# Kernel optimization log

Hardware: AMD Instinct MI355X
Metric: run time of the kernel (lower is better)

The kernel has to match this reference:

```python
import jax, jax.numpy as jnp
import numpy as np

B, W, C = 128, 64, 48
NUM_CHARS, E, H, HM, CTX, CTXM, OUT = 256, 64, 128, 128, 128, 128, 8


def _gru(x, lens, Wih, Whh, bih, bhh):
    """Masked unidirectional GRU. x: [N,T,D], lens: [N]. Outputs zero at t>=len
    (matching pad_packed_sequence), state frozen past len."""
    N, T, _ = x.shape
    Hd = Whh.shape[1]
    xg = jnp.einsum('ntd,gd->ntg', x, Wih) + bih  # [N,T,3H] precomputed input gates

    def step(h, inp):
        xg_t, t = inp
        hg = h @ Whh.T + bhh
        xr, xz, xn = jnp.split(xg_t, 3, axis=-1)
        hr, hz, hn = jnp.split(hg, 3, axis=-1)
        r = jax.nn.sigmoid(xr + hr)
        z = jax.nn.sigmoid(xz + hz)
        n = jnp.tanh(xn + r * hn)
        hnew = (1 - z) * n + z * h
        valid = (t < lens)[:, None]
        h2 = jnp.where(valid, hnew, h)
        out = jnp.where(valid, hnew, jnp.zeros_like(hnew))
        return h2, out

    h0 = jnp.zeros((N, Hd), x.dtype)
    _, outs = jax.lax.scan(step, h0, (xg.transpose(1, 0, 2), jnp.arange(T)))
    return outs.transpose(1, 0, 2)  # [N,T,H]


def _rev(x, lens):
    """Reverse each sequence within its valid length; pad positions unchanged."""
    T = x.shape[1]
    t = jnp.arange(T)[None, :]
    idx = jnp.where(t < lens[:, None], lens[:, None] - 1 - t, t)
    return jnp.take_along_axis(x, idx[:, :, None], axis=1)


def _bigru(x, lens, Wf, Uf, bif, bhf, Wb, Ub, bib, bhb):
    of = _gru(x, lens, Wf, Uf, bif, bhf)
    ob = _rev(_gru(_rev(x, lens), lens, Wb, Ub, bib, bhb), lens)
    return jnp.concatenate([of, ob], axis=-1)


def _attn_pool(out, Wp, bp, ctx):
    # out: [N,T,K]; softmax over ALL T positions (pads have out=0, faithful to source)
    proj = jnp.tanh(jnp.einsum('ntk,ck->ntc', out, Wp) + bp)
    att = jax.nn.softmax(proj @ ctx, axis=1)  # [N,T]
    return jnp.einsum('nt,ntk->nk', att, out)


def setup_inputs():
    key = jax.random.key(0)
    ks = iter(jax.random.split(key, 40))
    nrm = lambda shape: jax.random.normal(next(ks), shape, jnp.float32) * 0.1
    chars = jax.random.randint(next(ks), (B, W, C), 0, NUM_CHARS, dtype=jnp.int32)
    lens = jax.random.randint(next(ks), (B, W), 1, C + 1, dtype=jnp.int32)
    inp = dict(chars=chars, lens=lens, emb=nrm((NUM_CHARS, E)))
    for p, din, h in [('c', E, H), ('m', 2 * H, HM)]:
        for d in ('f', 'b'):
            inp[p + 'Wih_' + d] = nrm((3 * h, din))
            inp[p + 'Whh_' + d] = nrm((3 * h, h))
            inp[p + 'bih_' + d] = nrm((3 * h,))
            inp[p + 'bhh_' + d] = nrm((3 * h,))
    inp.update(wWp=nrm((CTX, 2 * H)), wbp=nrm((CTX,)), wctx=nrm((CTX,)),
               pWp=nrm((CTXM, 2 * HM)), pbp=nrm((CTXM,)), pctx=nrm((CTXM,)),
               Wout=nrm((OUT, 2 * HM)), bout=nrm((OUT,)))
    return inp


def reference(chars, lens, emb,
              cWih_f, cWhh_f, cbih_f, cbhh_f, cWih_b, cWhh_b, cbih_b, cbhh_b,
              mWih_f, mWhh_f, mbih_f, mbhh_f, mWih_b, mWhh_b, mbih_b, mbhh_b,
              wWp, wbp, wctx, pWp, pbp, pctx, Wout, bout):
    Bb, Ww, Cc = chars.shape
    x = emb[chars.reshape(Bb * Ww, Cc)]        # [B*W, C, E]
    l = lens.reshape(Bb * Ww)
    char_out = _bigru(x, l, cWih_f, cWhh_f, cbih_f, cbhh_f,
                      cWih_b, cWhh_b, cbih_b, cbhh_b)  # [B*W, C, 2H]
    words = _attn_pool(char_out, wWp, wbp, wctx).reshape(Bb, Ww, -1)  # [B, W, 2H]
    lw = jnp.full((Bb,), Ww, dtype=lens.dtype)
    msg_out = _bigru(words, lw, mWih_f, mWhh_f, mbih_f, mbhh_f,
                     mWih_b, mWhh_b, mbih_b, mbhh_b)  # [B, W, 2HM]
    messages = _attn_pool(msg_out, pWp, pbp, pctx)     # [B, 2HM]
    outputs = messages @ Wout.T + bout                 # [B, OUT]
    return outputs, messages
```

## Files before the change

### kernel.cpp

```cpp
#include <hip/hip_runtime.h>
#include <stdint.h>
#include <stddef.h>

#define NCH   256
#define EDIM  64
#define HDIM  128
#define G3    384
#define BATCH 128
#define WRD   64
#define CLEN  48
#define NW    8192
#define OUTD  8

#define LOG2E 1.44269504088896f

#define C_EMB     0
#define C_CWIH_F  16384
#define C_CWHH_F  40960
#define C_CBIH_F  90112
#define C_CBHH_F  90496
#define C_CWIH_B  90880
#define C_CWHH_B  115456
#define C_CBIH_B  164608
#define C_CBHH_B  164992
#define C_MWIH_F  165376
#define C_MWHH_F  263680
#define C_MBIH_F  312832
#define C_MBHH_F  313600
#define C_MWIH_B  314368
#define C_MWHH_B  412672
#define C_MBIH_B  461824
#define C_MBHH_B  462592
#define C_WWP     463360
#define C_WBP     496128
#define C_WCTX    496256
#define C_PWP     496384
#define C_PBP     529152
#define C_PCTX    529280
#define C_WOUT    529408
#define C_BOUT    531456
#define C_TOTAL   531464

#define OFF_FLAG    0u
#define OFF_CANON   1024u
#define OFF_WPFRAG  (4u*1024u*1024u)
#define OFF_PFRAG   (4u*1024u*1024u + 65536u)
#define OFF_MFRAG   (4u*1024u*1024u + 131072u)
#define OFF_BIASV   (4u*1024u*1024u + 524288u)
#define OFF_XGT4    5111808u
#define OFF_WORDS   35651584u
#define OFF_MSGOUT  47185920u
#define OFF_CHOUT   54525952u

typedef _Float16 h2v __attribute__((ext_vector_type(2)));
typedef _Float16 f16x8 __attribute__((ext_vector_type(8)));
typedef float f32x4 __attribute__((ext_vector_type(4)));

__device__ __forceinline__ float bf16_to_f32(unsigned short u){
  union{unsigned int i;float f;}v; v.i=((unsigned int)u)<<16; return v.f;
}
__device__ __forceinline__ unsigned short f32_to_bf16(float f){
  union{float f;unsigned int i;}v; v.f=f;
  unsigned int u=v.i; unsigned int r=(u + 0x7fffu + ((u>>16)&1u))>>16;
  return (unsigned short)r;
}
__device__ __forceinline__ uint32_t pack_h2(float x,float y){
  h2v h; h[0]=(_Float16)x; h[1]=(_Float16)y; uint32_t u; __builtin_memcpy(&u,&h,4); return u;
}
__device__ __forceinline__ unsigned short f32_to_h16u(float f){
  _Float16 h=(_Float16)f; unsigned short u; __builtin_memcpy(&u,&h,2); return u;
}
__device__ __forceinline__ float dot2(uint32_t a, uint32_t b, float c){
#if __has_builtin(__builtin_amdgcn_fdot2)
  h2v av,bv; __builtin_memcpy(&av,&a,4); __builtin_memcpy(&bv,&b,4);
  return __builtin_amdgcn_fdot2(av,bv,c,false);
#else
  h2v av,bv; __builtin_memcpy(&av,&a,4); __builtin_memcpy(&bv,&b,4);
  return c + (float)av[0]*(float)bv[0] + (float)av[1]*(float)bv[1];
#endif
}
__device__ __forceinline__ float exp2_fast(float x){
#if __has_builtin(__builtin_amdgcn_exp2f)
  return __builtin_amdgcn_exp2f(x);
#else
  return exp2f(x);
#endif
}
__device__ __forceinline__ float rcp_fast(float x){
#if __has_builtin(__builtin_amdgcn_rcpf)
  return __builtin_amdgcn_rcpf(x);
#else
  return 1.f/x;
#endif
}
__device__ __forceinline__ float sig2(float s){ return rcp_fast(1.f+exp2_fast(s)); }
__device__ __forceinline__ float tanh2(float u){ return fmaf(-2.f, rcp_fast(exp2_fast(u)+1.f), 1.f); }
__device__ __forceinline__ float wave_sum(float v){
  #pragma unroll
  for(int m=32;m>=1;m>>=1) v += __shfl_xor(v,m,64);
  return v;
}
__device__ __forceinline__ float wave_max(float v){
  #pragma unroll
  for(int m=32;m>=1;m>>=1) v = fmaxf(v,__shfl_xor(v,m,64));
  return v;
}
__device__ __forceinline__ f32x4 mfma16(f16x8 a, f16x8 b, f32x4 c){
  return __builtin_amdgcn_mfma_f32_16x16x32_f16(a, b, c, 0, 0, 0);
}

struct ConvArgs { const void* src[25]; int len[25]; int off[25]; };

__global__ void k_convert(ConvArgs a, int* __restrict__ flag, float* __restrict__ dst){
  const unsigned short* u=(const unsigned short*)a.src[0];
  int found=0;
  for(int i=threadIdx.x;i<2048;i+=256){ float v=bf16_to_f32(u[i]); if(fabsf(v)>8.f) found=1; }
  __shared__ int s;
  if(threadIdx.x==0) s=0;
  __syncthreads();
  if(found) atomicOr(&s,1);
  __syncthreads();
  int isf32=s;
  if(blockIdx.x==0 && threadIdx.x==0) *flag=isf32;
  int idx=blockIdx.x*256+threadIdx.x;
  #pragma unroll 1
  for(int i=0;i<25;i++){
    if(idx < a.len[i]){
      float v = isf32 ? ((const float*)a.src[i])[idx]
                      : bf16_to_f32(((const unsigned short*)a.src[i])[idx]);
      dst[a.off[i]+idx]=v;
      return;
    }
    idx -= a.len[i];
  }
}

__global__ void k_prep(const float* __restrict__ cw, unsigned short* __restrict__ wpfrag,
                       unsigned short* __restrict__ pfrag, unsigned short* __restrict__ mfrag,
                       float* __restrict__ biasv){
  int idx=blockIdx.x*256+threadIdx.x;
  if(idx<32768){
    int j=idx&7, lane=(idx>>3)&63, nt=(idx>>9)&7, ks=idx>>12;
    int nl=lane&15, q=lane>>4;
    float v = cw[C_WWP + (nt*16+nl)*256 + ks*32 + q*8 + j] * (2.f*LOG2E);
    wpfrag[idx]=f32_to_h16u(v);
  } else if(idx<65536){
    int i=idx-32768;
    int j=i&7, lane=(i>>3)&63, nt=(i>>9)&7, ks=i>>12;
    int nl=lane&15, q=lane>>4;
    float v = cw[C_PWP + (nt*16+nl)*256 + ks*32 + q*8 + j] * (2.f*LOG2E);
    pfrag[i]=f32_to_h16u(v);
  } else if(idx<262144){
    int i=idx-65536;
    int j=i&7, lane=(i>>3)&63, t2=i>>9;
    int nt=t2%48, ks=t2/48;
    int n=nt*16+(lane&15), k=ks*32+(lane>>4)*8+j;
    int gate = (n<G3)? n : n-G3;
    float sc = (gate<256)? -LOG2E : 2.f*LOG2E;
    float v = ((n<G3)? cw[C_MWIH_F + n*256 + k] : cw[C_MWIH_B + (n-G3)*256 + k]) * sc;
    mfrag[i]=f32_to_h16u(v);
  } else if(idx<262912){
    int i=idx-262144;
    int dir=i/384, g=i-384*(i/384);
    float b = cw[(dir?C_MBIH_B:C_MBIH_F)+g] + ((g<256)? cw[(dir?C_MBHH_B:C_MBHH_F)+g] : 0.f);
    biasv[i] = b * ((g<256)? -LOG2E : 2.f*LOG2E);
  }
}

__global__ __launch_bounds__(512) void k_prepx(const float* __restrict__ cw,
                                               float4* __restrict__ xgt4){
  int tid=threadIdx.x;
  int w=tid>>6, L=tid&63, nl=L&15, q=L>>4;
  int mchunk=blockIdx.x, dir=blockIdx.y;
  const float* Wih=cw+(dir?C_CWIH_B:C_CWIH_F);
  const float* bih=cw+(dir?C_CBIH_B:C_CBIH_F);
  const float* bhh=cw+(dir?C_CBHH_B:C_CBHH_F);
  int c16=w*16+nl;

  f16x8 bw[3][2];
  #pragma unroll
  for(int i=0;i<3;i++){
    int n=(w+8*i)*16+nl;
    const float* wr=Wih + n*EDIM;
    #pragma unroll
    for(int ks=0;ks<2;ks++){
      const float4* p=(const float4*)(wr + ks*32 + q*8);
      float4 v0=p[0], v1=p[1];
      f16x8 f;
      f[0]=(_Float16)v0.x; f[1]=(_Float16)v0.y; f[2]=(_Float16)v0.z; f[3]=(_Float16)v0.w;
      f[4]=(_Float16)v1.x; f[5]=(_Float16)v1.y; f[6]=(_Float16)v1.z; f[7]=(_Float16)v1.w;
      bw[i][ks]=f;
    }
  }
  float br=bih[c16]+bhh[c16];
  float bz=bih[128+c16]+bhh[128+c16];
  float bn=bih[256+c16];

  #pragma unroll
  for(int mt=0;mt<2;mt++){
    int ch=mchunk*32+mt*16+nl;
    f32x4 ar={0,0,0,0}, az={0,0,0,0}, an={0,0,0,0};
    #pragma unroll
    for(int ks=0;ks<2;ks++){
      const float4* p=(const float4*)(cw + C_EMB + ch*EDIM + ks*32 + q*8);
      float4 v0=p[0], v1=p[1];
      f16x8 a;
      a[0]=(_Float16)v0.x; a[1]=(_Float16)v0.y; a[2]=(_Float16)v0.z; a[3]=(_Float16)v0.w;
      a[4]=(_Float16)v1.x; a[5]=(_Float16)v1.y; a[6]=(_Float16)v1.z; a[7]=(_Float16)v1.w;
      ar=mfma16(a,bw[0][ks],ar); az=mfma16(a,bw[1][ks],az); an=mfma16(a,bw[2][ks],an);
    }
    #pragma unroll
    for(int r=0;r<4;r++){
      int chr=mchunk*32+mt*16+q*4+r;
      xgt4[dir*32768 + chr*128 + c16] =
        make_float4((ar[r]+br)*(-LOG2E), (az[r]+bz)*(-LOG2E), (an[r]+bn)*(2.f*LOG2E), 0.f);
    }
  }
}

__global__ __launch_bounds__(512,4) void k_chargru(const int* __restrict__ chars,
    const int* __restrict__ lensp, const float* __restrict__ cw,
    const float4* __restrict__ xgt4, unsigned short* __restrict__ chout){
  int tid=threadIdx.x;
  int w=tid>>6, L=tid&63, nl=L&15, q=L>>4;
  int dir=blockIdx.y;
  int seq0=blockIdx.x*16;
  const float* Whh=cw+(dir?C_CWHH_B:C_CWHH_F);
  const float* bhh=cw+(dir?C_CBHH_B:C_CBHH_F);
  const float4* xg4 = xgt4 + (dir<<15);

  int c16=w*16+nl;
  f16x8 bh[3][4];
  const float wsc[3]={-LOG2E,-LOG2E,2.f*LOG2E};
  #pragma unroll
  for(int i=0;i<3;i++){
    int n=(w+8*i)*16+nl;
    const float* wr=Whh + n*HDIM;
    float sc=wsc[i];
    #pragma unroll
    for(int c=0;c<4;c++){
      const float4* p=(const float4*)(wr + c*32 + q*8);
      float4 v0=p[0], v1=p[1];
      f16x8 f;
      f[0]=(_Float16)(v0.x*sc); f[1]=(_Float16)(v0.y*sc); f[2]=(_Float16)(v0.z*sc); f[3]=(_Float16)(v0.w*sc);
      f[4]=(_Float16)(v1.x*sc); f[5]=(_Float16)(v1.y*sc); f[6]=(_Float16)(v1.z*sc); f[7]=(_Float16)(v1.w*sc);
      bh[i][c]=f;
    }
  }
  float bias_hn=bhh[256+c16]*(2.f*LOG2E);

  __shared__ int cidT[CLEN][16];
  __shared__ int lenS[16];
  __shared__ __align__(16) _Float16 hbuf[2][16][136];

  for(int i=tid;i<16*CLEN;i+=512){ int t=i>>4, s=i&15; cidT[t][s]=chars[(seq0+s)*CLEN+t]; }
  if(tid<16) lenS[tid]=lensp[seq0+tid];
  for(int i=tid;i<16*136/2;i+=512) ((uint32_t*)&hbuf[0][0][0])[i]=0u;
  __syncthreads();

  int lenq[4];
  #pragma unroll
  for(int r=0;r<4;r++) lenq[r]=lenS[q*4+r];
  int sw=tid>>5, aw=tid&31;
  int lenp=lenS[sw];

  float4 pf[4];
  {
    int t0 = dir ? CLEN-1 : 0;
    int4 c4=*(const int4*)&cidT[t0][q*4];
    pf[0]=xg4[c4.x*128+c16]; pf[1]=xg4[c4.y*128+c16];
    pf[2]=xg4[c4.z*128+c16]; pf[3]=xg4[c4.w*128+c16];
  }
  float hreg[4]={0.f,0.f,0.f,0.f};
  unsigned short* wp = chout + ((size_t)(seq0+sw)*CLEN + (dir?CLEN-1:0))*256 + dir*HDIM + 4*aw;
  int dstep = dir ? -256 : 256;

  for(int step=0; step<CLEN; ++step){
    int t = dir ? CLEN-1-step : step;
    int p = step&1;
    float4 qf[4];
    bool havepf = (step+1 < CLEN);
    if(havepf){
      int tn = dir ? CLEN-2-step : step+1;
      int4 c4=*(const int4*)&cidT[tn][q*4];
      qf[0]=xg4[c4.x*128+c16]; qf[1]=xg4[c4.y*128+c16];
      qf[2]=xg4[c4.z*128+c16]; qf[3]=xg4[c4.w*128+c16];
    }
    f32x4 ra={0,0,0,0}, rb={0,0,0,0}, za={0,0,0,0}, zb={0,0,0,0};
    f32x4 ha={bias_hn,bias_hn,bias_hn,bias_hn}, hb={0,0,0,0};
    const _Float16* hrow=&hbuf[p][nl][0];
    f16x8 af0=*(const f16x8*)(hrow + 0*32 + q*8);
    f16x8 af1=*(const f16x8*)(hrow + 1*32 + q*8);
    f16x8 af2=*(const f16x8*)(hrow + 2*32 + q*8);
    f16x8 af3=*(const f16x8*)(hrow + 3*32 + q*8);
    ra=mfma16(af0,bh[0][0],ra); za=mfma16(af0,bh[1][0],za); ha=mfma16(af0,bh[2][0],ha);
    rb=mfma16(af1,bh[0][1],rb); zb=mfma16(af1,bh[1][1],zb); hb=mfma16(af1,bh[2][1],hb);
    ra=mfma16(af2,bh[0][2],ra); za=mfma16(af2,bh[1][2],za); ha=mfma16(af2,bh[2][2],ha);
    rb=mfma16(af3,bh[0][3],rb); zb=mfma16(af3,bh[1][3],zb); hb=mfma16(af3,bh[2][3],hb);
    f32x4 accr=ra+rb, accz=za+zb, a2h=ha+hb;
    #pragma unroll
    for(int r=0;r<4;r++){
      float rg=sig2(accr[r]+pf[r].x);
      float zg=sig2(accz[r]+pf[r].y);
      float nn=tanh2(fmaf(rg,a2h[r],pf[r].z));
      float hnew=fmaf(zg,hreg[r]-nn,nn);
      bool valid = t < lenq[r];
      float hv = valid ? hnew : hreg[r];
      hreg[r]=hv;
      hbuf[p^1][q*4+r][c16]=(_Float16)hv;
    }
    __syncthreads();
    {
      uint2 d=*(const uint2*)&hbuf[p^1][sw][4*aw];
      if(t>=lenp){ d.x=0u; d.y=0u; }
      *(uint2*)wp = d;
      wp += dstep;
    }
    if(havepf){
      #pragma unroll
      for(int r=0;r<4;r++) pf[r]=qf[r];
    }
  }
}

__global__ __launch_bounds__(256,4) void k_wpool(const unsigned short* __restrict__ chout,
    const unsigned short* __restrict__ wpfrag, const float* __restrict__ bp,
    const float* __restrict__ ctxv, _Float16* __restrict__ wordsF16){
  int n=blockIdx.x, tid=threadIdx.x;
  int w=tid>>6, lane=tid&63, nl=lane&15, q=lane>>4;
  __shared__ __align__(16) _Float16 sa[48][264];
  __shared__ float redl[48][4];
  __shared__ float att[48];

  uint4 bfr[2][8];
  const uint4* wp4=(const uint4*)wpfrag;
  #pragma unroll
  for(int ks=0;ks<8;ks++){
    bfr[0][ks]=wp4[(ks*8+2*w  )*64+lane];
    bfr[1][ks]=wp4[(ks*8+2*w+1)*64+lane];
  }
  {
    const uint4* src=(const uint4*)(chout + (size_t)n*48*256);
    #pragma unroll
    for(int i=0;i<6;i++){
      int ii=tid+256*i; int row=ii>>5, c16=ii&31;
      *(uint4*)&sa[row][c16*8]=src[ii];
    }
  }
  __syncthreads();

  f32x4 acc[3][2];
  #pragma unroll
  for(int mt=0;mt<3;mt++){ acc[mt][0]=(f32x4){0,0,0,0}; acc[mt][1]=(f32x4){0,0,0,0}; }
  #pragma unroll
  for(int ks=0;ks<8;ks++){
    f16x8 b0,b1;
    __builtin_memcpy(&b0,&bfr[0][ks],16);
    __builtin_memcpy(&b1,&bfr[1][ks],16);
    #pragma unroll
    for(int mt=0;mt<3;mt++){
      f16x8 af=*(const f16x8*)&sa[mt*16+nl][ks*32+q*8];
      acc[mt][0]=mfma16(af,b0,acc[mt][0]);
      acc[mt][1]=mfma16(af,b1,acc[mt][1]);
    }
  }
  int c0=(2*w)*16+nl, c1=c0+16;
  float bp0=bp[c0]*(2.f*LOG2E), bp1=bp[c1]*(2.f*LOG2E);
  float cv0=ctxv[c0], cv1=ctxv[c1];
  #pragma unroll
  for(int mt=0;mt<3;mt++){
    #pragma unroll
    for(int r=0;r<4;r++){
      float v=tanh2(acc[mt][0][r]+bp0)*cv0 + tanh2(acc[mt][1][r]+bp1)*cv1;
      v+=__shfl_xor(v,1,64); v+=__shfl_xor(v,2,64);
      v+=__shfl_xor(v,4,64); v+=__shfl_xor(v,8,64);
      if(nl==0) redl[mt*16+q*4+r][w]=v;
    }
  }
  __syncthreads();
  if(tid<64){
    float v=(tid<48)?(redl[tid][0]+redl[tid][1]+redl[tid][2]+redl[tid][3]):-1e30f;
    float mx=wave_max(v);
    float e=(tid<48)?exp2_fast((v-mx)*LOG2E):0.f;
    float s=wave_sum(e);
    if(tid<48) att[tid]=e*rcp_fast(s);
  }
  __syncthreads();
  float a=0.f;
  #pragma unroll 1
  for(int t=0;t<48;t++) a=fmaf(att[t],(float)sa[t][tid],a);
  wordsF16[(size_t)n*256+tid]=(_Float16)a;
}

__global__ __launch_bounds__(384) void k_msggru(const float* __restrict__ cw,
    const _Float16* __restrict__ wordsF16, const unsigned short* __restrict__ mfrag,
    const float* __restrict__ biasv, unsigned short* __restrict__ msg_out){
  int dir=blockIdx.y, b=blockIdx.x, tid=threadIdx.x;
  int w=tid>>6, lane=tid&63, nl=lane&15, q=lane>>4;

  __shared__ _Float16 xgL[64][392];
  __shared__ __align__(16) _Float16 hh[HDIM];
  __shared__ float rr[HDIM], zz[HDIM], xns[HDIM], hns[HDIM];

  {
    int ntb = dir*24 + w*4;
    const uint4* mf4=(const uint4*)mfrag;
    const uint4* wv=(const uint4*)wordsF16;
    f32x4 acc[4][4];
    #pragma unroll
    for(int mt=0;mt<4;mt++)
      #pragma unroll
      for(int i=0;i<4;i++) acc[mt][i]=(f32x4){0,0,0,0};
    #pragma unroll
    for(int ks=0;ks<8;ks++){
      f16x8 bf[4];
      #pragma unroll
      for(int i=0;i<4;i++){
        uint4 u=mf4[((ks*48 + ntb+i)*64 + lane)];
        __builtin_memcpy(&bf[i],&u,16);
      }
      #pragma unroll
      for(int mt=0;mt<4;mt++){
        uint4 u=wv[((size_t)b*64 + mt*16 + nl)*32 + ks*4 + q];
        f16x8 av; __builtin_memcpy(&av,&u,16);
        #pragma unroll
        for(int i=0;i<4;i++) acc[mt][i]=mfma16(av,bf[i],acc[mt][i]);
      }
    }
    float bi[4];
    #pragma unroll
    for(int i=0;i<4;i++) bi[i]=biasv[dir*384 + (w*4+i)*16+nl];
    #pragma unroll
    for(int mt=0;mt<4;mt++)
      #pragma unroll
      for(int i=0;i<4;i++){
        int g=(w*4+i)*16+nl;
        #pragma unroll
        for(int r=0;r<4;r++)
          xgL[mt*16+q*4+r][g]=(_Float16)(acc[mt][i][r]+bi[i]);
      }
  }

  const float* Whh=cw+(dir?C_MWHH_B:C_MWHH_F);
  const float* bhh=cw+(dir?C_MBHH_B:C_MBHH_F);
  uint32_t whh[64];
  {
    float sc = (tid<256) ? -LOG2E : 2.f*LOG2E;
    const float4* h4=(const float4*)(Whh + tid*HDIM);
    #pragma unroll
    for(int i=0;i<32;i++){ float4 v=h4[i]; whh[2*i]=pack_h2(v.x*sc,v.y*sc); whh[2*i+1]=pack_h2(v.z*sc,v.w*sc); }
  }
  float ha0 = (tid>=256) ? bhh[tid]*(2.f*LOG2E) : 0.f;
  if(tid<64) ((uint32_t*)hh)[tid]=0u;
  float hreg=0.f;
  __syncthreads();
  int j=tid&127, gt=tid>>7;
  for(int step=0;step<WRD;step++){
    int wt = dir ? (WRD-1-step) : step;
    float xacc = (float)xgL[wt][tid];
    float ha=ha0;
    const uint4* hp=(const uint4*)hh;
    #pragma unroll
    for(int qq=0;qq<16;qq++){ uint4 v=hp[qq];
      ha=dot2(whh[4*qq+0],v.x,ha); ha=dot2(whh[4*qq+1],v.y,ha);
      ha=dot2(whh[4*qq+2],v.z,ha); ha=dot2(whh[4*qq+3],v.w,ha); }
    if(gt==0)      rr[j]=sig2(xacc+ha);
    else if(gt==1) zz[j]=sig2(xacc+ha);
    else { xns[j]=xacc; hns[j]=ha; }
    __syncthreads();
    if(tid<HDIM){
      float r=rr[tid], z=zz[tid];
      float nn=tanh2(fmaf(r,hns[tid],xns[tid]));
      float hnew=fmaf(z,hreg-nn,nn);
      hreg=hnew;
      hh[tid]=(_Float16)hnew;
      msg_out[(size_t)(b*WRD+wt)*256 + dir*HDIM + tid]=f32_to_h16u(hnew);
    }
    __syncthreads();
  }
}

__global__ __launch_bounds__(256) void k_mpool(const unsigned short* __restrict__ outp,
    const unsigned short* __restrict__ pfrag, const float* __restrict__ bp,
    const float* __restrict__ ctxv,
    const float* __restrict__ Wout, const float* __restrict__ bout,
    void* dout, const int* __restrict__ flag){
  int n=blockIdx.x, tid=threadIdx.x;
  int w=tid>>6, lane=tid&63, nl=lane&15, q=lane>>4;
  __shared__ __align__(16) _Float16 sa[64][264];
  __shared__ float redl[64][4];
  __shared__ float att[64];
  __shared__ float msgv[256];

  uint4 bfr[2][8];
  const uint4* pf4=(const uint4*)pfrag;
  #pragma unroll
  for(int ks=0;ks<8;ks++){
    bfr[0][ks]=pf4[(ks*8+2*w  )*64+lane];
    bfr[1][ks]=pf4[(ks*8+2*w+1)*64+lane];
  }
  {
    const uint4* src=(const uint4*)(outp + (size_t)n*64*256);
    #pragma unroll
    for(int i=0;i<8;i++){
      int ii=tid+256*i; int row=ii>>5, c16=ii&31;
      *(uint4*)&sa[row][c16*8]=src[ii];
    }
  }
  __syncthreads();

  f32x4 acc[4][2];
  #pragma unroll
  for(int mt=0;mt<4;mt++){ acc[mt][0]=(f32x4){0,0,0,0}; acc[mt][1]=(f32x4){0,0,0,0}; }
  #pragma unroll
  for(int ks=0;ks<8;ks++){
    f16x8 b0,b1;
    __builtin_memcpy(&b0,&bfr[0][ks],16);
    __builtin_memcpy(&b1,&bfr[1][ks],16);
    #pragma unroll
    for(int mt=0;mt<4;mt++){
      f16x8 af=*(const f16x8*)&sa[mt*16+nl][ks*32+q*8];
      acc[mt][0]=mfma16(af,b0,acc[mt][0]);
      acc[mt][1]=mfma16(af,b1,acc[mt][1]);
    }
  }
  int c0=(2*w)*16+nl, c1=c0+16;
  float bp0=bp[c0]*(2.f*LOG2E), bp1=bp[c1]*(2.f*LOG2E);
  float cv0=ctxv[c0], cv1=ctxv[c1];
  #pragma unroll
  for(int mt=0;mt<4;mt++){
    #pragma unroll
    for(int r=0;r<4;r++){
      float v=tanh2(acc[mt][0][r]+bp0)*cv0 + tanh2(acc[mt][1][r]+bp1)*cv1;
      v+=__shfl_xor(v,1,64); v+=__shfl_xor(v,2,64);
      v+=__shfl_xor(v,4,64); v+=__shfl_xor(v,8,64);
      if(nl==0) redl[mt*16+q*4+r][w]=v;
    }
  }
  __syncthreads();
  if(tid<64){
    float v=redl[tid][0]+redl[tid][1]+redl[tid][2]+redl[tid][3];
    float mx=wave_max(v);
    float e=exp2_fast((v-mx)*LOG2E);
    float s=wave_sum(e);
    att[tid]=e*rcp_fast(s);
  }
  __syncthreads();
  float a=0.f;
  #pragma unroll 1
  for(int t=0;t<64;t++) a=fmaf(att[t],(float)sa[t][tid],a);
  msgv[tid]=a;
  if(*flag){ ((float*)dout)[1024 + n*256 + tid]=a; }
  else { ((unsigned short*)dout)[1024 + n*256 + tid]=f32_to_bf16(a); }
  __syncthreads();
  if(tid<OUTD){
    float acc2=bout[tid];
    #pragma unroll 1
    for(int k=0;k<256;k++) acc2=fmaf(msgv[k], Wout[tid*256+k], acc2);
    if(*flag) ((float*)dout)[n*OUTD+tid]=acc2;
    else ((unsigned short*)dout)[n*OUTD+tid]=f32_to_bf16(acc2);
  }
}

extern "C" void kernel_launch(void* const* d_in, const int* in_sizes, int n_in,
                              void* d_out, int out_size, void* d_ws, size_t ws_size,
                              hipStream_t stream){
  (void)in_sizes; (void)n_in; (void)out_size; (void)ws_size;
  char* ws=(char*)d_ws;
  int* flag=(int*)(ws+OFF_FLAG);
  float* canon=(float*)(ws+OFF_CANON);
  unsigned short* wpfrag=(unsigned short*)(ws+OFF_WPFRAG);
  unsigned short* pfrag=(unsigned short*)(ws+OFF_PFRAG);
  unsigned short* mfrag=(unsigned short*)(ws+OFF_MFRAG);
  float* biasv=(float*)(ws+OFF_BIASV);
  float4* xgt4=(float4*)(ws+OFF_XGT4);
  _Float16* wordsF16=(_Float16*)(ws+OFF_WORDS);
  unsigned short* msgout=(unsigned short*)(ws+OFF_MSGOUT);
  unsigned short* chout=(unsigned short*)(ws+OFF_CHOUT);
  const int* chars=(const int*)d_in[0];
  const int* lensp=(const int*)d_in[1];

  ConvArgs ca;
  static const int clen_[25]={16384,24576,49152,384,384,24576,49152,384,384,
                              98304,49152,768,768,98304,49152,768,768,
                              32768,128,128,32768,128,128,2048,8};
  int off=0;
  for(int i=0;i<25;i++){ ca.src[i]=d_in[i+2]; ca.len[i]=clen_[i]; ca.off[i]=off; off+=clen_[i]; }
  hipLaunchKernelGGL(k_convert, dim3((C_TOTAL+255)/256), dim3(256), 0, stream, ca, flag, canon);
  hipLaunchKernelGGL(k_prep, dim3(1028), dim3(256), 0, stream, canon, wpfrag, pfrag, mfrag, biasv);
  hipLaunchKernelGGL(k_prepx, dim3(8,2), dim3(512), 0, stream, canon, xgt4);
  hipLaunchKernelGGL(k_chargru, dim3(NW/16,2), dim3(512), 0, stream, chars, lensp, canon, xgt4, chout);
  hipLaunchKernelGGL(k_wpool, dim3(NW), dim3(256), 0, stream, chout, wpfrag,
                     canon+C_WBP, canon+C_WCTX, wordsF16);
  hipLaunchKernelGGL(k_msggru, dim3(BATCH,2), dim3(384), 0, stream, canon, wordsF16, mfrag, biasv, msgout);
  hipLaunchKernelGGL(k_mpool, dim3(BATCH), dim3(256), 0, stream, msgout, pfrag,
                     canon+C_PBP, canon+C_PCTX,
                     canon+C_WOUT, canon+C_BOUT, d_out, flag);
}
```

Measured before the change: 406.4 us.

## Sort char sequences by length and skip padded steps in GRU and pooling

Adds a one-block counting sort that orders the 8192 words by descending length. Each char-GRU block of 16 sequences then runs only up to its group's maximum length instead of the full 48 steps, and pad rows are no longer written. The word-pooling kernel loads and multiplies only valid rows and fills pad positions with a precomputed constant logit (tanh(bp)·ctx), which matches zero outputs at pads. The cost is an extra serial sort launch, an indirect gather through the order array, and reliance on the unwritten pad rows never being read.

```diff
diff --git a/kernel.cpp b/kernel.cpp
--- a/kernel.cpp
+++ b/kernel.cpp
@@ -47,6 +47,7 @@
 #define OFF_PFRAG   (4u*1024u*1024u + 65536u)
 #define OFF_MFRAG   (4u*1024u*1024u + 131072u)
 #define OFF_BIASV   (4u*1024u*1024u + 524288u)
+#define OFF_ORD     (4u*1024u*1024u + 532480u)
 #define OFF_XGT4    5111808u
 #define OFF_WORDS   35651584u
 #define OFF_MSGOUT  47185920u
@@ -132,6 +133,23 @@
       return;
     }
     idx -= a.len[i];
+  }
+}
+
+__global__ void k_sort(const int* __restrict__ lensp, int* __restrict__ ord){
+  __shared__ int hist[64];
+  __shared__ int base[64];
+  int tid=threadIdx.x;
+  if(tid<64) hist[tid]=0;
+  __syncthreads();
+  for(int i=tid;i<NW;i+=256) atomicAdd(&hist[48-lensp[i]],1);
+  __syncthreads();
+  if(tid==0){ int s=0; for(int b=0;b<64;b++){ base[b]=s; s+=hist[b]; } }
+  __syncthreads();
+  for(int i=tid;i<NW;i+=256){
+    int b=48-lensp[i];
+    int pos=atomicAdd(&base[b],1);
+    ord[pos]=i;
   }
 }
 
@@ -164,6 +182,10 @@
     int dir=i/384, g=i-384*(i/384);
     float b = cw[(dir?C_MBIH_B:C_MBIH_F)+g] + ((g<256)? cw[(dir?C_MBHH_B:C_MBHH_F)+g] : 0.f);
     biasv[i] = b * ((g<256)? -LOG2E : 2.f*LOG2E);
+  } else if(idx==262912){
+    float a=0.f;
+    for(int c=0;c<128;c++) a += tanh2(cw[C_WBP+c]*(2.f*LOG2E))*cw[C_WCTX+c];
+    biasv[768]=a;
   }
 }
 
@@ -219,8 +241,9 @@
 }
 
 __global__ __launch_bounds__(512,4) void k_chargru(const int* __restrict__ chars,
-    const int* __restrict__ lensp, const float* __restrict__ cw,
-    const float4* __restrict__ xgt4, unsigned short* __restrict__ chout){
+    const int* __restrict__ lensp, const int* __restrict__ ord,
+    const float* __restrict__ cw, const float4* __restrict__ xgt4,
+    unsigned short* __restrict__ chout){
   int tid=threadIdx.x;
   int w=tid>>6, L=tid&63, nl=L&15, q=L>>4;
   int dir=blockIdx.y;
@@ -249,39 +272,46 @@
   }
   float bias_hn=bhh[256+c16]*(2.f*LOG2E);
 
+  __shared__ int sord[16];
   __shared__ int cidT[CLEN][16];
   __shared__ int lenS[16];
   __shared__ __align__(16) _Float16 hbuf[2][16][136];
 
-  for(int i=tid;i<16*CLEN;i+=512){ int t=i>>4, s=i&15; cidT[t][s]=chars[(seq0+s)*CLEN+t]; }
-  if(tid<16) lenS[tid]=lensp[seq0+tid];
+  if(tid<16) sord[tid]=ord[seq0+tid];
+  __syncthreads();
+  for(int i=tid;i<16*CLEN;i+=512){ int t=i>>4, s=i&15; cidT[t][s]=chars[sord[s]*CLEN+t]; }
+  if(tid<16) lenS[tid]=lensp[sord[tid]];
   for(int i=tid;i<16*136/2;i+=512) ((uint32_t*)&hbuf[0][0][0])[i]=0u;
   __syncthreads();
 
+  int maxlen=1;
+  #pragma unroll 1
+  for(int s=0;s<16;s++) maxlen=max(maxlen,lenS[s]);
   int lenq[4];
   #pragma unroll
   for(int r=0;r<4;r++) lenq[r]=lenS[q*4+r];
   int sw=tid>>5, aw=tid&31;
   int lenp=lenS[sw];
+  int sq=sord[sw];
 
   float4 pf[4];
   {
-    int t0 = dir ? CLEN-1 : 0;
+    int t0 = dir ? maxlen-1 : 0;
     int4 c4=*(const int4*)&cidT[t0][q*4];
     pf[0]=xg4[c4.x*128+c16]; pf[1]=xg4[c4.y*128+c16];
     pf[2]=xg4[c4.z*128+c16]; pf[3]=xg4[c4.w*128+c16];
   }
   float hreg[4]={0.f,0.f,0.f,0.f};
-  unsigned short* wp = chout + ((size_t)(seq0+sw)*CLEN + (dir?CLEN-1:0))*256 + dir*HDIM + 4*aw;
+  unsigned short* wp = chout + ((size_t)sq*CLEN + (dir?maxlen-1:0))*256 + dir*HDIM + 4*aw;
   int dstep = dir ? -256 : 256;
 
-  for(int step=0; step<CLEN; ++step){
-    int t = dir ? CLEN-1-step : step;
+  for(int step=0; step<maxlen; ++step){
+    int t = dir ? maxlen-1-step : step;
     int p = step&1;
     float4 qf[4];
-    bool havepf = (step+1 < CLEN);
+    bool havepf = (step+1 < maxlen);
     if(havepf){
-      int tn = dir ? CLEN-2-step : step+1;
+      int tn = dir ? maxlen-2-step : step+1;
       int4 c4=*(const int4*)&cidT[tn][q*4];
       qf[0]=xg4[c4.x*128+c16]; qf[1]=xg4[c4.y*128+c16];
       qf[2]=xg4[c4.z*128+c16]; qf[3]=xg4[c4.w*128+c16];
@@ -310,12 +340,11 @@
       hbuf[p^1][q*4+r][c16]=(_Float16)hv;
     }
     __syncthreads();
-    {
+    if(t<lenp){
       uint2 d=*(const uint2*)&hbuf[p^1][sw][4*aw];
-      if(t>=lenp){ d.x=0u; d.y=0u; }
       *(uint2*)wp = d;
-      wp += dstep;
-    }
+    }
+    wp += dstep;
     if(havepf){
       #pragma unroll
       for(int r=0;r<4;r++) pf[r]=qf[r];
@@ -325,9 +354,12 @@
 
 __global__ __launch_bounds__(256,4) void k_wpool(const unsigned short* __restrict__ chout,
     const unsigned short* __restrict__ wpfrag, const float* __restrict__ bp,
-    const float* __restrict__ ctxv, _Float16* __restrict__ wordsF16){
+    const float* __restrict__ ctxv, const int* __restrict__ lensp,
+    const float* __restrict__ L0p, _Float16* __restrict__ wordsF16){
   int n=blockIdx.x, tid=threadIdx.x;
   int w=tid>>6, lane=tid&63, nl=lane&15, q=lane>>4;
+  int len=lensp[n];
+  float L0=*L0p;
   __shared__ __align__(16) _Float16 sa[48][264];
   __shared__ float redl[48][4];
   __shared__ float att[48];
@@ -341,14 +373,15 @@
   }
   {
     const uint4* src=(const uint4*)(chout + (size_t)n*48*256);
-    #pragma unroll
-    for(int i=0;i<6;i++){
-      int ii=tid+256*i; int row=ii>>5, c16=ii&31;
+    #pragma unroll 1
+    for(int ii=tid; ii<len*32; ii+=256){
+      int row=ii>>5, c16=ii&31;
       *(uint4*)&sa[row][c16*8]=src[ii];
     }
   }
   __syncthreads();
 
+  int mtmax=(len+15)>>4;
   f32x4 acc[3][2];
   #pragma unroll
   for(int mt=0;mt<3;mt++){ acc[mt][0]=(f32x4){0,0,0,0}; acc[mt][1]=(f32x4){0,0,0,0}; }
@@ -359,9 +392,11 @@
     __builtin_memcpy(&b1,&bfr[1][ks],16);
     #pragma unroll
     for(int mt=0;mt<3;mt++){
-      f16x8 af=*(const f16x8*)&sa[mt*16+nl][ks*32+q*8];
-      acc[mt][0]=mfma16(af,b0,acc[mt][0]);
-      acc[mt][1]=mfma16(af,b1,acc[mt][1]);
+      if(mt<mtmax){
+        f16x8 af=*(const f16x8*)&sa[mt*16+nl][ks*32+q*8];
+        acc[mt][0]=mfma16(af,b0,acc[mt][0]);
+        acc[mt][1]=mfma16(af,b1,acc[mt][1]);
+      }
     }
   }
   int c0=(2*w)*16+nl, c1=c0+16;
@@ -369,17 +404,22 @@
   float cv0=ctxv[c0], cv1=ctxv[c1];
   #pragma unroll
   for(int mt=0;mt<3;mt++){
-    #pragma unroll
-    for(int r=0;r<4;r++){
-      float v=tanh2(acc[mt][0][r]+bp0)*cv0 + tanh2(acc[mt][1][r]+bp1)*cv1;
-      v+=__shfl_xor(v,1,64); v+=__shfl_xor(v,2,64);
-      v+=__shfl_xor(v,4,64); v+=__shfl_xor(v,8,64);
-      if(nl==0) redl[mt*16+q*4+r][w]=v;
+    if(mt<mtmax){
+      #pragma unroll
+      for(int r=0;r<4;r++){
+        float v=tanh2(acc[mt][0][r]+bp0)*cv0 + tanh2(acc[mt][1][r]+bp1)*cv1;
+        v+=__shfl_xor(v,1,64); v+=__shfl_xor(v,2,64);
+        v+=__shfl_xor(v,4,64); v+=__shfl_xor(v,8,64);
+        if(nl==0) redl[mt*16+q*4+r][w]=v;
+      }
     }
   }
   __syncthreads();
   if(tid<64){
-    float v=(tid<48)?(redl[tid][0]+redl[tid][1]+redl[tid][2]+redl[tid][3]):-1e30f;
+    float v;
+    if(tid<len) v=redl[tid][0]+redl[tid][1]+redl[tid][2]+redl[tid][3];
+    else if(tid<48) v=L0;
+    else v=-1e30f;
     float mx=wave_max(v);
     float e=(tid<48)?exp2_fast((v-mx)*LOG2E):0.f;
     float s=wave_sum(e);
@@ -388,7 +428,7 @@
   __syncthreads();
   float a=0.f;
   #pragma unroll 1
-  for(int t=0;t<48;t++) a=fmaf(att[t],(float)sa[t][tid],a);
+  for(int t=0;t<len;t++) a=fmaf(att[t],(float)sa[t][tid],a);
   wordsF16[(size_t)n*256+tid]=(_Float16)a;
 }
 
@@ -573,6 +613,7 @@
   unsigned short* pfrag=(unsigned short*)(ws+OFF_PFRAG);
   unsigned short* mfrag=(unsigned short*)(ws+OFF_MFRAG);
   float* biasv=(float*)(ws+OFF_BIASV);
+  int* ord=(int*)(ws+OFF_ORD);
   float4* xgt4=(float4*)(ws+OFF_XGT4);
   _Float16* wordsF16=(_Float16*)(ws+OFF_WORDS);
   unsigned short* msgout=(unsigned short*)(ws+OFF_MSGOUT);
@@ -587,11 +628,12 @@
   int off=0;
   for(int i=0;i<25;i++){ ca.src[i]=d_in[i+2]; ca.len[i]=clen_[i]; ca.off[i]=off; off+=clen_[i]; }
   hipLaunchKernelGGL(k_convert, dim3((C_TOTAL+255)/256), dim3(256), 0, stream, ca, flag, canon);
+  hipLaunchKernelGGL(k_sort, dim3(1), dim3(256), 0, stream, lensp, ord);
   hipLaunchKernelGGL(k_prep, dim3(1028), dim3(256), 0, stream, canon, wpfrag, pfrag, mfrag, biasv);
   hipLaunchKernelGGL(k_prepx, dim3(8,2), dim3(512), 0, stream, canon, xgt4);
-  hipLaunchKernelGGL(k_chargru, dim3(NW/16,2), dim3(512), 0, stream, chars, lensp, canon, xgt4, chout);
+  hipLaunchKernelGGL(k_chargru, dim3(NW/16,2), dim3(512), 0, stream, chars, lensp, ord, canon, xgt4, chout);
   hipLaunchKernelGGL(k_wpool, dim3(NW), dim3(256), 0, stream, chout, wpfrag,
-                     canon+C_WBP, canon+C_WCTX, wordsF16);
+                     canon+C_WBP, canon+C_WCTX, lensp, biasv+768, wordsF16);
   hipLaunchKernelGGL(k_msggru, dim3(BATCH,2), dim3(384), 0, stream, canon, wordsF16, mfrag, biasv, msgout);
   hipLaunchKernelGGL(k_mpool, dim3(BATCH), dim3(256), 0, stream, msgout, pfrag,
                      canon+C_PBP, canon+C_PCTX,
```

New measurement: 506.8 us. 1.25x slower.
